# Kernel tuning notes

Measured on AMD Instinct MI355X. Metric: run time of the kernel, lower is better.

The kernel has to match this reference:

```python
import jax, jax.numpy as jnp
import numpy as np

B, N, D, C, H, W = 4, 900, 256, 256, 200, 200
HEADS, LVLS, PTS, K = 8, 1, 4, 10


def setup_inputs() -> dict:
    key = jax.random.key(0)
    ks = jax.random.split(key, 16)
    s = 0.02
    return {
        "query_embed": jax.random.normal(ks[0], (B, N, D), jnp.float32),
        "ctrl_points": jax.random.uniform(ks[1], (B, N, 4, 2), jnp.float32, -50.0, 50.0),
        "bev_features": jax.random.normal(ks[2], (B, C, H, W), jnp.float32),
        "spatial_shapes": jnp.array([[H, W]], dtype=jnp.int32),
        "pc_range": jnp.array([-51.2, -51.2, -5.0, 51.2, 51.2, 3.0], jnp.float32),
        "Wq": s * jax.random.normal(ks[3], (D, D)), "bq": jnp.zeros((D,)),
        "Wv": s * jax.random.normal(ks[4], (C, D)), "bv": jnp.zeros((D,)),
        "Woff": s * jax.random.normal(ks[5], (D, HEADS * LVLS * PTS * 2)), "boff": jnp.zeros((HEADS * LVLS * PTS * 2,)),
        "Wattn": s * jax.random.normal(ks[6], (D, HEADS * LVLS * PTS)), "battn": jnp.zeros((HEADS * LVLS * PTS,)),
        "Wmo": s * jax.random.normal(ks[7], (D, D)), "bmo": jnp.zeros((D,)),
        "Wo": s * jax.random.normal(ks[8], (D, D)), "bo": jnp.zeros((D,)),
    }


def _forward(query_embed, ctrl_points, bev_features, spatial_shapes, pc_range,
             Wq, bq, Wv, bv, Woff, boff, Wattn, battn, Wmo, bmo, Wo, bo):
    b, n, d = query_embed.shape
    _, c, h, w = bev_features.shape
    hd = d // HEADS

    # --- cubic Bezier interpolation: (B,N,4,2) -> (B,N,K,2) dense points ---
    t = jnp.linspace(0.0, 1.0, K, dtype=query_embed.dtype)
    basis = jnp.stack([(1 - t) ** 3, 3 * (1 - t) ** 2 * t, 3 * (1 - t) * t ** 2, t ** 3], axis=-1)  # (K,4)
    dense = jnp.einsum('kc,bncd->bnkd', basis, ctrl_points)
    # --- normalize to [0,1] by pc_range, clamp to [0.01,0.99] ---
    nx = (dense[..., 0] - pc_range[0]) / (pc_range[3] - pc_range[0])
    ny = (dense[..., 1] - pc_range[1]) / (pc_range[4] - pc_range[1])
    ref = jnp.clip(jnp.stack([nx, ny], axis=-1), 0.01, 0.99)  # (B,N,K,2)

    # --- projections ---
    q = query_embed @ Wq + bq                                       # (B,N,D) (identity for residual)
    v = bev_features.reshape(b, c, h * w).transpose(0, 2, 1) @ Wv + bv  # (B,HW,D)
    v = v.reshape(b, h * w, HEADS, hd)

    off = (q @ Woff + boff).reshape(b, n, HEADS, LVLS, PTS, 2)
    aw = jax.nn.softmax((q @ Wattn + battn).reshape(b, n, HEADS, LVLS * PTS), axis=-1)
    aw = aw.reshape(b, n, HEADS, PTS)  # LVLS == 1

    # offset normalizer = (W, H) per level
    normalizer = jnp.stack([spatial_shapes[..., 1], spatial_shapes[..., 0]], axis=-1).astype(q.dtype)  # (L,2)
    # sampling locations: broadcast K bezier points against heads/points offsets
    loc = ref[:, :, None, :, None, :] + off / normalizer[None, None, None, :, None, :]  # (B,N,HEADS,K,PTS,2)

    # --- bilinear sampling, align_corners=False, zero padding ---
    gx = loc[..., 0] * w - 0.5
    gy = loc[..., 1] * h - 0.5
    x0 = jnp.floor(gx)
    y0 = jnp.floor(gy)
    wx = gx - x0
    wy = gy - y0
    x0i = x0.astype(jnp.int32)
    y0i = y0.astype(jnp.int32)

    vflat = v.transpose(0, 2, 1, 3).reshape(b * HEADS, h * w, hd)  # (B*HEADS, HW, hd)

    def flat(a):  # (B,N,HEADS,K,PTS) -> (B*HEADS, N*K*PTS)
        return a.transpose(0, 2, 1, 3, 4).reshape(b * HEADS, n * K * PTS)

    acc = jnp.zeros((b * HEADS, n * K * PTS, hd), dtype=q.dtype)
    for dx, dy in ((0, 0), (1, 0), (0, 1), (1, 1)):
        ix = flat(x0i) + dx
        iy = flat(y0i) + dy
        wxx = flat(wx) if dx else (1.0 - flat(wx))
        wyy = flat(wy) if dy else (1.0 - flat(wy))
        valid = (ix >= 0) & (ix < w) & (iy >= 0) & (iy < h)
        idx = jnp.clip(iy, 0, h - 1) * w + jnp.clip(ix, 0, w - 1)
        corner = jnp.take_along_axis(vflat, idx[..., None], axis=1)  # (B*HEADS, Npts, hd)
        acc = acc + corner * (wxx * wyy * valid.astype(q.dtype))[..., None]

    sampled = acc.reshape(b, HEADS, n, K, PTS, hd)
    # weighted sum over (K, PTS); attention weights shared across the K bezier points
    out = jnp.einsum('bhnkpd,bnhp->bnhd', sampled, aw).reshape(b, n, d)
    out = out @ Wmo + bmo + q   # mmcv MSDeformAttn output_proj + residual (identity = query)
    out = out @ Wo + bo         # outer output_proj
    return out


def reference(query_embed, ctrl_points, bev_features, spatial_shapes, pc_range,
              Wq, bq, Wv, bv, Woff, boff, Wattn, battn, Wmo, bmo, Wo, bo):
    return _forward(query_embed, ctrl_points, bev_features, spatial_shapes, pc_range,
                    Wq, bq, Wv, bv, Woff, boff, Wattn, battn, Wmo, bmo, Wo, bo)
```

## Files before the change

kernel.cpp:

```cpp
#include <hip/hip_runtime.h>
#include <hip/hip_bf16.h>
#include <math.h>


typedef unsigned short u16;
typedef unsigned int u32;
typedef short bf16x8 __attribute__((ext_vector_type(8)));
typedef float f32x4 __attribute__((ext_vector_type(4)));

__device__ __forceinline__ float bflo(u32 w) {
  union { u32 i; float f; } c; c.i = w << 16; return c.f;
}
__device__ __forceinline__ float bfhi(u32 w) {
  union { u32 i; float f; } c; c.i = w & 0xffff0000u; return c.f;
}
__device__ __forceinline__ u16 f2bf(float f) {
  union { float f; u32 i; } c; c.f = f;
  u32 u = c.i;
  return (u16)((u + 0x7FFFu + ((u >> 16) & 1u)) >> 16);
}
__device__ __forceinline__ int imin(int a, int b) { return a < b ? a : b; }
__device__ __forceinline__ int imax(int a, int b) { return a > b ? a : b; }

__device__ __forceinline__ void glds16(const u16* g, u16* l) {
  __builtin_amdgcn_global_load_lds(
      (__attribute__((address_space(1))) const void*)g,
      (__attribute__((address_space(3))) void*)l, 16, 0, 0);
}

__global__ __launch_bounds__(256) void prep_weights(
    const float* __restrict__ Wq, const float* __restrict__ Wv,
    const float* __restrict__ Woff, const float* __restrict__ Wattn,
    const float* __restrict__ Wmo, const float* __restrict__ Wo,
    const float* __restrict__ bq, const float* __restrict__ boff,
    const float* __restrict__ battn, const float* __restrict__ bmo,
    const float* __restrict__ bo, const float* __restrict__ query,
    u16* __restrict__ bqoaT, u16* __restrict__ wvT, u16* __restrict__ woCat,
    float* __restrict__ bcat, float* __restrict__ bprime,
    u16* __restrict__ qin)
{
  const int idx = blockIdx.x * 256 + threadIdx.x;
  {
    int i = idx * 4;
    float4 v = *(const float4*)(query + i);
    uint2 st;
    st.x = (u32)f2bf(v.x) | ((u32)f2bf(v.y) << 16);
    st.y = (u32)f2bf(v.z) | ((u32)f2bf(v.w) << 16);
    *(uint2*)(qin + i) = st;
  }
  if (idx < 65536) {
    int r = idx >> 8, c = idx & 255;
    bqoaT[idx] = f2bf(Wq[c * 256 + r]);
    wvT[idx]   = f2bf(Wv[c * 256 + r]);
  }
  if (idx < 24576) {
    int n = idx >> 8, k = idx & 255;
    const float* wq = Wq + k * 256;
    float s = 0.f;
    if (n < 64) {
      const float* wo = Woff + n;
#pragma unroll 4
      for (int c = 0; c < 256; c += 4) {
        float4 a = *(const float4*)(wq + c);
        s += a.x * wo[(c + 0) * 64] + a.y * wo[(c + 1) * 64] +
             a.z * wo[(c + 2) * 64] + a.w * wo[(c + 3) * 64];
      }
    } else {
      const float* wa = Wattn + (n - 64);
#pragma unroll 4
      for (int c = 0; c < 256; c += 4) {
        float4 a = *(const float4*)(wq + c);
        s += a.x * wa[(c + 0) * 32] + a.y * wa[(c + 1) * 32] +
             a.z * wa[(c + 2) * 32] + a.w * wa[(c + 3) * 32];
      }
    }
    bqoaT[65536 + idx] = f2bf(s);
  }
  if (idx < 131072) {
    int n = idx >> 9, k = idx & 511;
    float s;
    if (k >= 256) {
      s = Wo[(size_t)(k - 256) * 256 + n];
    } else {
      const float* wm = Wmo + k * 256;
      const float* wo = Wo + n;
      s = 0.f;
#pragma unroll 4
      for (int c = 0; c < 256; c += 4) {
        float4 a = *(const float4*)(wm + c);
        s += a.x * wo[(c + 0) * 256] + a.y * wo[(c + 1) * 256] +
             a.z * wo[(c + 2) * 256] + a.w * wo[(c + 3) * 256];
      }
    }
    woCat[idx] = f2bf(s);
  }
  if (idx >= 131072 && idx < 131328) {
    int n = idx - 131072;
    const float* wo = Wo + n;
    float s = bo[n];
    for (int c = 0; c < 256; ++c) s += bmo[c] * wo[c * 256];
    bprime[n] = s;
  }
  if (idx >= 131328 && idx < 131680) {
    int n = idx - 131328;
    if (n < 256) {
      bcat[n] = bq[n];
    } else {
      int j = n - 256;
      float s;
      if (j < 64) {
        const float* wo = Woff + j;
        s = boff[j];
        for (int c = 0; c < 256; ++c) s += bq[c] * wo[c * 64];
      } else {
        const float* wa = Wattn + (j - 64);
        s = battn[j - 64];
        for (int c = 0; c < 256; ++c) s += bq[c] * wa[c * 32];
      }
      bcat[n] = s;
    }
  }
}

enum { GM_F32 = 0, GM_SPLIT = 1 };

template <int MODE>
__global__ __launch_bounds__(256) void gemm_bt(
    const u16* __restrict__ A, const u16* __restrict__ Bt,
    const float* __restrict__ bias,
    u16* __restrict__ outb, float* __restrict__ outf,
    int M, int N, int K, int lda, int ldo)
{
  __shared__ __align__(16) u16 lA[128 * 32];
  __shared__ __align__(16) u16 lB[128 * 32];
  const int tid = threadIdx.x;
  const int wv = tid >> 6, lane = tid & 63;
  const int m0 = blockIdx.y * 128;
  const int n0 = blockIdx.x * 128;

  const int crow = lane >> 2;
  const int ckoff = (lane & 3) * 8;
  const int a1 = imin(m0 + wv * 16 + crow, M - 1);
  const int a2 = imin(m0 + (wv + 4) * 16 + crow, M - 1);
  const int b1 = imin(n0 + wv * 16 + crow, N - 1);
  const int b2 = imin(n0 + (wv + 4) * 16 + crow, N - 1);
  const u16* gA1 = A + (size_t)a1 * lda + ckoff;
  const u16* gA2 = A + (size_t)a2 * lda + ckoff;
  const u16* gB1 = Bt + (size_t)b1 * K + ckoff;
  const u16* gB2 = Bt + (size_t)b2 * K + ckoff;
  u16* lA1 = lA + wv * 512;  u16* lA2 = lA + (wv + 4) * 512;
  u16* lB1 = lB + wv * 512;  u16* lB2 = lB + (wv + 4) * 512;

  const int fm = (wv & 1) * 64, fn = (wv >> 1) * 64;
  const int fr = lane & 15, fk = (lane >> 4) * 8;

  f32x4 acc[4][4];
#pragma unroll
  for (int i = 0; i < 4; ++i)
#pragma unroll
    for (int j = 0; j < 4; ++j) acc[i][j] = (f32x4){0.f, 0.f, 0.f, 0.f};

  for (int k0 = 0; k0 < K; k0 += 32) {
    glds16(gA1 + k0, lA1);
    glds16(gA2 + k0, lA2);
    glds16(gB1 + k0, lB1);
    glds16(gB2 + k0, lB2);
    __syncthreads();
    bf16x8 af[4], bfv[4];
#pragma unroll
    for (int i = 0; i < 4; ++i)
      af[i] = *(const bf16x8*)&lA[(fm + i * 16 + fr) * 32 + fk];
#pragma unroll
    for (int j = 0; j < 4; ++j)
      bfv[j] = *(const bf16x8*)&lB[(fn + j * 16 + fr) * 32 + fk];
    __syncthreads();
#pragma unroll
    for (int i = 0; i < 4; ++i)
#pragma unroll
      for (int j = 0; j < 4; ++j)
        acc[i][j] = __builtin_amdgcn_mfma_f32_16x16x32_bf16(af[i], bfv[j], acc[i][j], 0, 0, 0);
  }

  const int quad = lane >> 4;
#pragma unroll
  for (int j = 0; j < 4; ++j) {
    const int n = n0 + fn + j * 16 + fr;
    const bool nok = (n < N);
    const float bcol = bias[nok ? n : 0];
#pragma unroll
    for (int i = 0; i < 4; ++i) {
      const int mb = m0 + fm + i * 16 + quad * 4;
#pragma unroll
      for (int r = 0; r < 4; ++r) {
        const int m = mb + r;
        if (m < M && nok) {
          float x = acc[i][j][r] + bcol;
          if (MODE == GM_F32) {
            outf[(size_t)m * ldo + n] = x;
          } else {
            if (n < 256) outb[(size_t)m * 512 + n] = f2bf(x);
            else outf[(size_t)m * 96 + (n - 256)] = x;
          }
        }
      }
    }
  }
}

#define LOADB(S, R0, R1, R2, R3)                                   \
  { const float* s2_ = src + (size_t)((S) * 32) * 40000;           \
    R0 = *(const float4*)(s2_);                                    \
    R1 = *(const float4*)(s2_ + 4);                                \
    R2 = *(const float4*)(s2_ + 40000);                            \
    R3 = *(const float4*)(s2_ + 40004); }

#define CVW8(BUF, R0, R1, R2, R3)                                            \
  { u32* lbw_ = (u32*)(BUF); u32 pk_;                                        \
    asm("v_cvt_pk_bf16_f32 %0, %1, %2" : "=v"(pk_) : "v"(R0.x), "v"(R2.x)); \
    lbw_[(((wrow + 0) * 16 + wslot) ^ wxor)] = pk_;                          \
    asm("v_cvt_pk_bf16_f32 %0, %1, %2" : "=v"(pk_) : "v"(R0.y), "v"(R2.y)); \
    lbw_[(((wrow + 1) * 16 + wslot) ^ wxor)] = pk_;                          \
    asm("v_cvt_pk_bf16_f32 %0, %1, %2" : "=v"(pk_) : "v"(R0.z), "v"(R2.z)); \
    lbw_[(((wrow + 2) * 16 + wslot) ^ wxor)] = pk_;                          \
    asm("v_cvt_pk_bf16_f32 %0, %1, %2" : "=v"(pk_) : "v"(R0.w), "v"(R2.w)); \
    lbw_[(((wrow + 3) * 16 + wslot) ^ wxor)] = pk_;                          \
    asm("v_cvt_pk_bf16_f32 %0, %1, %2" : "=v"(pk_) : "v"(R1.x), "v"(R3.x)); \
    lbw_[(((wrow + 4) * 16 + wslot) ^ wxor)] = pk_;                          \
    asm("v_cvt_pk_bf16_f32 %0, %1, %2" : "=v"(pk_) : "v"(R1.y), "v"(R3.y)); \
    lbw_[(((wrow + 5) * 16 + wslot) ^ wxor)] = pk_;                          \
    asm("v_cvt_pk_bf16_f32 %0, %1, %2" : "=v"(pk_) : "v"(R1.z), "v"(R3.z)); \
    lbw_[(((wrow + 6) * 16 + wslot) ^ wxor)] = pk_;                          \
    asm("v_cvt_pk_bf16_f32 %0, %1, %2" : "=v"(pk_) : "v"(R1.w), "v"(R3.w)); \
    lbw_[(((wrow + 7) * 16 + wslot) ^ wxor)] = pk_; }

__global__ __launch_bounds__(256, 2) void gemm_v(
    const u16* __restrict__ A,
    const float* __restrict__ bev,
    const float* __restrict__ bias,
    u16* __restrict__ outb)
{
  __shared__ __align__(16) u16 lA[8 * 128 * 32];
  __shared__ __align__(16) u16 lB[2][128 * 32];
  const int tid = threadIdx.x;
  const int wv = tid >> 6, lane = tid & 63;
  const int m0 = blockIdx.x * 128;
  const int n0 = blockIdx.y * 128;
  const int z = blockIdx.z;

  const int crow = lane >> 2, ckoff = (lane & 3) * 8;
  const u16* gA1 = A + (size_t)(m0 + wv * 16 + crow) * 256 + ckoff;
  const u16* gA2 = A + (size_t)(m0 + (wv + 4) * 16 + crow) * 256 + ckoff;
  u16* lA1 = lA + wv * 512;
  u16* lA2 = lA + (wv + 4) * 512;

  const int kp = tid >> 4, nb = tid & 15;
  const int cb = imin(n0 + nb * 8, 40000 - 8);
  const float* src = bev + ((size_t)z * 256 + 2 * kp) * 40000 + cb;
  const int wslot = (((kp >> 2) ^ (nb & 3)) << 2) + (kp & 3);
  const int wxor = ((nb >> 2) & 1) << 4;
  const int wrow = nb * 8;

  const int fm = (wv & 1) * 64, fn = (wv >> 1) * 64;
  const int fr = lane & 15, fk = (lane >> 4) * 8;

  f32x4 acc[4][4];
#pragma unroll
  for (int i = 0; i < 4; ++i)
#pragma unroll
    for (int j = 0; j < 4; ++j) acc[i][j] = (f32x4){0.f, 0.f, 0.f, 0.f};

  float4 s0a, s0b, s0c, s0d, s1a, s1b, s1c, s1d;
  float4 s2a, s2b, s2c, s2d, s3a, s3b, s3c, s3d;

  LOADB(0, s0a, s0b, s0c, s0d);
#pragma unroll
  for (int s = 0; s < 8; ++s) {
    glds16(gA1 + s * 32, lA1 + s * 4096);
    glds16(gA2 + s * 32, lA2 + s * 4096);
  }
  LOADB(1, s1a, s1b, s1c, s1d);
  LOADB(2, s2a, s2b, s2c, s2d);
  LOADB(3, s3a, s3b, s3c, s3d);
  asm volatile("" ::: "memory");
  CVW8(lB[0], s0a, s0b, s0c, s0d);
  __syncthreads();

#pragma unroll
  for (int t = 0; t < 8; ++t) {
    bf16x8 af[4], bfv[4];
#pragma unroll
    for (int i = 0; i < 4; ++i)
      af[i] = *(const bf16x8*)&lA[t * 4096 + (fm + i * 16 + fr) * 32 + fk];
#pragma unroll
    for (int j = 0; j < 4; ++j) {
      const int n = fn + j * 16 + fr;
      const int pc = (((lane >> 4) ^ ((n >> 3) & 3)) << 3);
      const int ri = (n * 32 + pc) ^ (((n >> 5) & 1) << 5);
      bfv[j] = *(const bf16x8*)&lB[t & 1][ri];
    }
    if (t == 0)      { LOADB(4, s0a, s0b, s0c, s0d); }
    else if (t == 1) { LOADB(5, s1a, s1b, s1c, s1d); }
    else if (t == 2) { LOADB(6, s2a, s2b, s2c, s2d); }
    else if (t == 3) { LOADB(7, s3a, s3b, s3c, s3d); }
    if (t == 0)      { CVW8(lB[1], s1a, s1b, s1c, s1d); }
    else if (t == 1) { CVW8(lB[0], s2a, s2b, s2c, s2d); }
    else if (t == 2) { CVW8(lB[1], s3a, s3b, s3c, s3d); }
    else if (t == 3) { CVW8(lB[0], s0a, s0b, s0c, s0d); }
    else if (t == 4) { CVW8(lB[1], s1a, s1b, s1c, s1d); }
    else if (t == 5) { CVW8(lB[0], s2a, s2b, s2c, s2d); }
    else if (t == 6) { CVW8(lB[1], s3a, s3b, s3c, s3d); }
#pragma unroll
    for (int i = 0; i < 4; ++i)
#pragma unroll
      for (int j = 0; j < 4; ++j)
        acc[i][j] = __builtin_amdgcn_mfma_f32_16x16x32_bf16(af[i], bfv[j], acc[i][j], 0, 0, 0);
    if (t < 7) {
      __builtin_amdgcn_sched_barrier(0);
      asm volatile("s_waitcnt lgkmcnt(0)" ::: "memory");
      __builtin_amdgcn_sched_barrier(0);
      __builtin_amdgcn_s_barrier();
      __builtin_amdgcn_sched_barrier(0);
    }
  }

  const int quad = lane >> 4;
#pragma unroll
  for (int j = 0; j < 4; ++j) {
    const int n = n0 + fn + j * 16 + fr;
    if (n < 40000) {
#pragma unroll
      for (int i = 0; i < 4; ++i) {
        const int mb = m0 + fm + i * 16 + quad * 4;
        u16 u0 = f2bf(acc[i][j][0] + bias[mb + 0]);
        u16 u1 = f2bf(acc[i][j][1] + bias[mb + 1]);
        u16 u2 = f2bf(acc[i][j][2] + bias[mb + 2]);
        u16 u3 = f2bf(acc[i][j][3] + bias[mb + 3]);
        size_t off = (size_t)z * (8ull * 40000 * 32) +
                     (size_t)(mb >> 5) * (40000 * 32) + (size_t)n * 32 + (mb & 31);
        uint2 st; st.x = (u32)u0 | ((u32)u1 << 16); st.y = (u32)u2 | ((u32)u3 << 16);
        *(uint2*)(outb + off) = st;
      }
    }
  }
}

__global__ __launch_bounds__(256) void sampler(
    const float* __restrict__ ctrl,
    const float* __restrict__ pc,
    const float* __restrict__ oa_,
    const u16* __restrict__ v,
    u16* __restrict__ attn_out)
{
  __shared__ int   sX0[4][40], sY0[4][40];
  __shared__ float sWx[4][40], sWy[4][40], sAw[4][40];
  const int w = threadIdx.x >> 6, lane = threadIdx.x & 63;
  const int bh = blockIdx.x & 31;
  const int n = (blockIdx.x >> 5) * 4 + w;
  const int h = bh & 7, b = bh >> 3;
  const int row = b * 900 + n;

  if (lane < 40) {
    const int k = lane >> 2, p = lane & 3;
    const float t = (float)k * (1.0f / 9.0f), u = 1.f - t;
    const float c0 = u * u * u, c1 = 3.f * u * u * t, c2 = 3.f * u * t * t, c3 = t * t * t;
    const float* cp = ctrl + (size_t)row * 8;
    float cx = c0 * cp[0] + c1 * cp[2] + c2 * cp[4] + c3 * cp[6];
    float cy = c0 * cp[1] + c1 * cp[3] + c2 * cp[5] + c3 * cp[7];
    float nx = (cx - pc[0]) / (pc[3] - pc[0]);
    float ny = (cy - pc[1]) / (pc[4] - pc[1]);
    nx = fminf(fmaxf(nx, 0.01f), 0.99f);
    ny = fminf(fmaxf(ny, 0.01f), 0.99f);
    const float* oa = oa_ + (size_t)row * 96;
    float ox = oa[h * 8 + p * 2 + 0], oy = oa[h * 8 + p * 2 + 1];
    float l0 = oa[64 + h * 4 + 0], l1 = oa[64 + h * 4 + 1];
    float l2 = oa[64 + h * 4 + 2], l3 = oa[64 + h * 4 + 3];
    float mx = fmaxf(fmaxf(l0, l1), fmaxf(l2, l3));
    float e0 = __expf(l0 - mx), e1 = __expf(l1 - mx), e2 = __expf(l2 - mx), e3 = __expf(l3 - mx);
    float lp = (p == 0) ? l0 : (p == 1) ? l1 : (p == 2) ? l2 : l3;
    float aw = __expf(lp - mx) / (e0 + e1 + e2 + e3);
    float gx = (nx + ox * (1.f / 200.f)) * 200.f - 0.5f;
    float gy = (ny + oy * (1.f / 200.f)) * 200.f - 0.5f;
    float x0 = floorf(gx), y0 = floorf(gy);
    sX0[w][lane] = (int)x0; sY0[w][lane] = (int)y0;
    sWx[w][lane] = gx - x0; sWy[w][lane] = gy - y0; sAw[w][lane] = aw;
  }
  __syncthreads();

  const int sg = lane >> 3;
  const int ch0 = (lane & 7) * 4;
  const u16* vb = v + ((size_t)(b * 8 + h)) * (40000 * 32) + ch0;
  float a0 = 0.f, a1 = 0.f, a2 = 0.f, a3 = 0.f;
#pragma unroll
  for (int p = 0; p < 5; ++p) {
    const int s = p * 8 + sg;
    const int x0 = sX0[w][s], y0 = sY0[w][s];
    const float wx = sWx[w][s], wy = sWy[w][s], aw = sAw[w][s];
    const int x1 = x0 + 1, y1 = y0 + 1;
    const int cx0 = imin(imax(x0, 0), 199), cx1 = imin(imax(x1, 0), 199);
    const int cy0 = imin(imax(y0, 0), 199), cy1 = imin(imax(y1, 0), 199);
    const bool vx0 = (u32)x0 < 200u, vx1 = (u32)x1 < 200u;
    const bool vy0 = (u32)y0 < 200u, vy1 = (u32)y1 < 200u;
    const float w00 = (vx0 && vy0) ? aw * (1.f - wx) * (1.f - wy) : 0.f;
    const float w10 = (vx1 && vy0) ? aw * wx * (1.f - wy) : 0.f;
    const float w01 = (vx0 && vy1) ? aw * (1.f - wx) * wy : 0.f;
    const float w11 = (vx1 && vy1) ? aw * wx * wy : 0.f;
    uint2 d00 = *(const uint2*)(vb + (size_t)(cy0 * 200 + cx0) * 32);
    uint2 d10 = *(const uint2*)(vb + (size_t)(cy0 * 200 + cx1) * 32);
    uint2 d01 = *(const uint2*)(vb + (size_t)(cy1 * 200 + cx0) * 32);
    uint2 d11 = *(const uint2*)(vb + (size_t)(cy1 * 200 + cx1) * 32);
    a0 += w00 * bflo(d00.x) + w10 * bflo(d10.x) + w01 * bflo(d01.x) + w11 * bflo(d11.x);
    a1 += w00 * bfhi(d00.x) + w10 * bfhi(d10.x) + w01 * bfhi(d01.x) + w11 * bfhi(d11.x);
    a2 += w00 * bflo(d00.y) + w10 * bflo(d10.y) + w01 * bflo(d01.y) + w11 * bflo(d11.y);
    a3 += w00 * bfhi(d00.y) + w10 * bfhi(d10.y) + w01 * bfhi(d01.y) + w11 * bfhi(d11.y);
  }
#pragma unroll
  for (int off = 8; off < 64; off <<= 1) {
    a0 += __shfl_xor(a0, off);
    a1 += __shfl_xor(a1, off);
    a2 += __shfl_xor(a2, off);
    a3 += __shfl_xor(a3, off);
  }
  if (lane < 8) {
    uint2 st;
    st.x = (u32)f2bf(a0) | ((u32)f2bf(a1) << 16);
    st.y = (u32)f2bf(a2) | ((u32)f2bf(a3) << 16);
    *(uint2*)(attn_out + (size_t)row * 512 + h * 32 + ch0) = st;
  }
}

extern "C" void kernel_launch(void* const* d_in, const int* in_sizes, int n_in,
                              void* d_out, int out_size, void* d_ws, size_t ws_size,
                              hipStream_t stream)
{
  const float* query = (const float*)d_in[0];
  const float* ctrl  = (const float*)d_in[1];
  const float* bev   = (const float*)d_in[2];
  const float* pc    = (const float*)d_in[4];
  const float* Wq    = (const float*)d_in[5];  const float* bq    = (const float*)d_in[6];
  const float* Wv    = (const float*)d_in[7];  const float* bv    = (const float*)d_in[8];
  const float* Woff  = (const float*)d_in[9];  const float* boff  = (const float*)d_in[10];
  const float* Wattn = (const float*)d_in[11]; const float* battn = (const float*)d_in[12];
  const float* Wmo   = (const float*)d_in[13]; const float* bmo   = (const float*)d_in[14];
  const float* Wo    = (const float*)d_in[15]; const float* bo    = (const float*)d_in[16];

  char* ws = (char*)d_ws;
  size_t off = 0;
  auto alloc = [&](size_t bytes) -> void* {
    void* p = ws + off; off += (bytes + 255) & ~(size_t)255; return p;
  };
  u16*  v     = (u16*)alloc(4ull * 8 * 40000 * 32 * 2);
  u16*  qin   = (u16*)alloc(3600ull * 256 * 2);
  u16*  wvT   = (u16*)alloc(65536 * 2);
  u16*  bqoaT = (u16*)alloc(352 * 256 * 2);
  u16*  woCat = (u16*)alloc(256 * 512 * 2);
  float* bcat = (float*)alloc(352 * 4);
  float* bprime = (float*)alloc(256 * 4);
  float* oaf  = (float*)alloc(3600ull * 96 * 4);
  u16*  qcat  = (u16*)alloc(3600ull * 512 * 2);
  (void)ws_size; (void)in_sizes; (void)n_in; (void)out_size;

  prep_weights<<<900, 256, 0, stream>>>(Wq, Wv, Woff, Wattn, Wmo, Wo,
                                        bq, boff, battn, bmo, bo, query,
                                        bqoaT, wvT, woCat, bcat, bprime, qin);
  gemm_v<<<dim3(2, 313, 4), 256, 0, stream>>>(wvT, bev, bv, v);
  gemm_bt<GM_SPLIT><<<dim3(3, 29), 256, 0, stream>>>(
      qin, bqoaT, bcat, qcat + 256, oaf, 3600, 352, 256, 256, 0);
  sampler<<<7200, 256, 0, stream>>>(ctrl, pc, oaf, v, qcat);
  gemm_bt<GM_F32><<<dim3(2, 29), 256, 0, stream>>>(
      qcat, woCat, bprime, nullptr, (float*)d_out, 3600, 256, 512, 512, 256);
}
```

Before: 384.0 us.

## Add LDS-free per-wave V projection kernel for half the batches

Introduces gemm_v4, where each wave computes all 256 output channels for 32 spatial columns. B is loaded straight from global memory into registers and converted to bf16 in-register, with no LDS staging or barriers. The original tiled LDS kernel is kept for batches 2-3 through a new zbase parameter. This removes shared-memory traffic and synchronisation, at the cost of strided global loads, repeated A fetches from cache, and large accumulator register use.

```diff
diff --git a/kernel.cpp b/kernel.cpp
--- a/kernel.cpp
+++ b/kernel.cpp
@@ -214,7 +214,7 @@
     R2 = *(const float4*)(s2_ + 40000);                            \
     R3 = *(const float4*)(s2_ + 40004); }
 
-#define CVW8(BUF, R0, R1, R2, R3)                                            \
+#define CVW8F(BUF, R0, R1, R2, R3)                                           \
   { u32* lbw_ = (u32*)(BUF); u32 pk_;                                        \
     asm("v_cvt_pk_bf16_f32 %0, %1, %2" : "=v"(pk_) : "v"(R0.x), "v"(R2.x)); \
     lbw_[(((wrow + 0) * 16 + wslot) ^ wxor)] = pk_;                          \
@@ -233,11 +233,78 @@
     asm("v_cvt_pk_bf16_f32 %0, %1, %2" : "=v"(pk_) : "v"(R1.w), "v"(R3.w)); \
     lbw_[(((wrow + 7) * 16 + wslot) ^ wxor)] = pk_; }
 
-__global__ __launch_bounds__(256, 2) void gemm_v(
+__global__ __launch_bounds__(256) void gemm_v4(
     const u16* __restrict__ A,
     const float* __restrict__ bev,
     const float* __restrict__ bias,
-    u16* __restrict__ outb)
+    u16* __restrict__ outb,
+    int zbase)
+{
+  const int tid = threadIdx.x;
+  const int wv = tid >> 6, lane = tid & 63;
+  const int z = zbase + blockIdx.y;
+  const int w = blockIdx.x * 4 + wv;
+  if (w >= 1250) return;
+  const int nw0 = w * 32;
+  const int fr = lane & 15, fk = (lane >> 4) * 8;
+
+  const float* bsrc = bev + ((size_t)z * 256 + fk) * 40000 + nw0 + fr;
+  const u16* asrc = A + (size_t)fr * 256 + fk;
+
+  f32x4 acc[16][2];
+#pragma unroll
+  for (int i = 0; i < 16; ++i) {
+    acc[i][0] = (f32x4){0.f, 0.f, 0.f, 0.f};
+    acc[i][1] = (f32x4){0.f, 0.f, 0.f, 0.f};
+  }
+
+#pragma unroll
+  for (int t = 0; t < 8; ++t) {
+    const float* bs = bsrc + (size_t)(t * 32) * 40000;
+    float b0[8], b1[8];
+#pragma unroll
+    for (int j = 0; j < 8; ++j) {
+      b0[j] = bs[(size_t)j * 40000];
+      b1[j] = bs[(size_t)j * 40000 + 16];
+    }
+    union { u32 u[4]; bf16x8 v; } p0, p1;
+#pragma unroll
+    for (int j = 0; j < 4; ++j) {
+      asm("v_cvt_pk_bf16_f32 %0, %1, %2"
+          : "=v"(p0.u[j]) : "v"(b0[2 * j]), "v"(b0[2 * j + 1]));
+      asm("v_cvt_pk_bf16_f32 %0, %1, %2"
+          : "=v"(p1.u[j]) : "v"(b1[2 * j]), "v"(b1[2 * j + 1]));
+    }
+#pragma unroll
+    for (int i = 0; i < 16; ++i) {
+      bf16x8 af = *(const bf16x8*)(asrc + i * 4096 + t * 32);
+      acc[i][0] = __builtin_amdgcn_mfma_f32_16x16x32_bf16(af, p0.v, acc[i][0], 0, 0, 0);
+      acc[i][1] = __builtin_amdgcn_mfma_f32_16x16x32_bf16(af, p1.v, acc[i][1], 0, 0, 0);
+    }
+  }
+
+  const int quad = lane >> 4;
+#pragma unroll
+  for (int i = 0; i < 16; ++i) {
+    const int mb = i * 16 + quad * 4;
+#pragma unroll
+    for (int j = 0; j < 2; ++j) {
+      const int n = nw0 + j * 16 + fr;
+      u16 u0 = f2bf(acc[i][j][0] + bias[mb + 0]);
+      u16 u1 = f2bf(acc[i][j][1] + bias[mb + 1]);
+      u16 u2 = f2bf(acc[i][j][2] + bias[mb + 2]);
+      u16 u3 = f2bf(acc[i][j][3] + bias[mb + 3]);
+      size_t off = (size_t)z * (8ull * 40000 * 32) +
+                   (size_t)(mb >> 5) * (40000 * 32) + (size_t)n * 32 + (mb & 31);
+      uint2 st; st.x = (u32)u0 | ((u32)u1 << 16); st.y = (u32)u2 | ((u32)u3 << 16);
+      *(uint2*)(outb + off) = st;
+    }
+  }
+}
+
+__global__ __launch_bounds__(256, 2) void gemm_v(
+    const u16* __restrict__ A, const float* __restrict__ bev,
+    const float* __restrict__ bias, u16* __restrict__ outb, int zbase)
 {
   __shared__ __align__(16) u16 lA[8 * 128 * 32];
   __shared__ __align__(16) u16 lB[2][128 * 32];
@@ -245,7 +312,7 @@
   const int wv = tid >> 6, lane = tid & 63;
   const int m0 = blockIdx.x * 128;
   const int n0 = blockIdx.y * 128;
-  const int z = blockIdx.z;
+  const int z = zbase + blockIdx.z;
 
   const int crow = lane >> 2, ckoff = (lane & 3) * 8;
   const u16* gA1 = A + (size_t)(m0 + wv * 16 + crow) * 256 + ckoff;
@@ -282,7 +349,7 @@
   LOADB(2, s2a, s2b, s2c, s2d);
   LOADB(3, s3a, s3b, s3c, s3d);
   asm volatile("" ::: "memory");
-  CVW8(lB[0], s0a, s0b, s0c, s0d);
+  CVW8F(lB[0], s0a, s0b, s0c, s0d);
   __syncthreads();
 
 #pragma unroll
@@ -302,13 +369,13 @@
     else if (t == 1) { LOADB(5, s1a, s1b, s1c, s1d); }
     else if (t == 2) { LOADB(6, s2a, s2b, s2c, s2d); }
     else if (t == 3) { LOADB(7, s3a, s3b, s3c, s3d); }
-    if (t == 0)      { CVW8(lB[1], s1a, s1b, s1c, s1d); }
-    else if (t == 1) { CVW8(lB[0], s2a, s2b, s2c, s2d); }
-    else if (t == 2) { CVW8(lB[1], s3a, s3b, s3c, s3d); }
-    else if (t == 3) { CVW8(lB[0], s0a, s0b, s0c, s0d); }
-    else if (t == 4) { CVW8(lB[1], s1a, s1b, s1c, s1d); }
-    else if (t == 5) { CVW8(lB[0], s2a, s2b, s2c, s2d); }
-    else if (t == 6) { CVW8(lB[1], s3a, s3b, s3c, s3d); }
+    if (t == 0)      { CVW8F(lB[1], s1a, s1b, s1c, s1d); }
+    else if (t == 1) { CVW8F(lB[0], s2a, s2b, s2c, s2d); }
+    else if (t == 2) { CVW8F(lB[1], s3a, s3b, s3c, s3d); }
+    else if (t == 3) { CVW8F(lB[0], s0a, s0b, s0c, s0d); }
+    else if (t == 4) { CVW8F(lB[1], s1a, s1b, s1c, s1d); }
+    else if (t == 5) { CVW8F(lB[0], s2a, s2b, s2c, s2d); }
+    else if (t == 6) { CVW8F(lB[1], s3a, s3b, s3c, s3d); }
 #pragma unroll
     for (int i = 0; i < 4; ++i)
 #pragma unroll
@@ -462,7 +529,8 @@
   prep_weights<<<900, 256, 0, stream>>>(Wq, Wv, Woff, Wattn, Wmo, Wo,
                                         bq, boff, battn, bmo, bo, query,
                                         bqoaT, wvT, woCat, bcat, bprime, qin);
-  gemm_v<<<dim3(2, 313, 4), 256, 0, stream>>>(wvT, bev, bv, v);
+  gemm_v4<<<dim3(313, 2), 256, 0, stream>>>(wvT, bev, bv, v, 0);
+  gemm_v<<<dim3(2, 313, 2), 256, 0, stream>>>(wvT, bev, bv, v, 2);
   gemm_bt<GM_SPLIT><<<dim3(3, 29), 256, 0, stream>>>(
       qin, bqoaT, bcat, qcat + 256, oaf, 3600, 352, 256, 256, 0);
   sampler<<<7200, 256, 0, stream>>>(ctrl, pc, oaf, v, qcat);
```

Result: slower. 437.6 us (+13.9%).
